# Optimization experiments

Measured on AMD Instinct MI355X. Metric: run time of the kernel, lower is better.

The kernel has to match this reference:

```python
import jax, jax.numpy as jnp
import numpy as np
import math

B, NQ, NK = 4, 2048, 2048
D = 1024          # dimension_k == dimension_v == dimension_q
H, DK, DV = 8, 128, 128
DO = 1024


def setup_inputs() -> dict:
    key = jax.random.key(0)
    ks = jax.random.split(key, 12)
    s = 0.02
    return {
        "q": jax.random.normal(ks[0], (B, NQ, D), jnp.float32),
        "k": jax.random.normal(ks[1], (B, NK, D), jnp.float32),
        "v": jax.random.normal(ks[2], (B, NK, D), jnp.float32),
        "mask": jax.random.normal(ks[3], (B, NQ, NK), jnp.float32),
        "Wq": jax.random.normal(ks[4], (H * DK, D), jnp.float32) * s,
        "bq": jnp.zeros((H * DK,), jnp.float32),
        "Wk": jax.random.normal(ks[5], (DK, D), jnp.float32) * s,
        "bk": jnp.zeros((DK,), jnp.float32),
        "Wv": jax.random.normal(ks[6], (DV, D), jnp.float32) * s,
        "bv": jnp.zeros((DV,), jnp.float32),
        "Wo": jax.random.normal(ks[7], (DO, H * DV), jnp.float32) * s,
        "bo": jnp.zeros((DO,), jnp.float32),
    }


def reference(q, k, v, mask, Wq, bq, Wk, bk, Wv, bv, Wo, bo):
    # projections
    qh = (q @ Wq.T + bq).reshape(B, NQ, H, DK)   # per-head queries
    kh = k @ Wk.T + bk                            # (B, NK, DK) shared across heads (MQA)
    vh = v @ Wv.T + bv                            # (B, NK, DV)
    # scores: shared K broadcast over heads instead of torch's repeat()
    att = jnp.einsum("bqhd,bkd->bhqk", qh, kh) / math.sqrt(DK)
    att = att + mask[:, None, :, :]
    att = jax.nn.softmax(att, axis=-1)
    outh = jnp.einsum("bhqk,bkd->bqhd", att, vh).reshape(B, NQ, H * DV)
    out = outh @ Wo.T + bo
    # original returns attention flattened head-major: (H*B, NQ, NK)
    attention = jnp.transpose(att, (1, 0, 2, 3)).reshape(H * B, NQ, NK)
    return attention, out
```

## Files before the change

kernel.cpp:

```cpp
#include <hip/hip_runtime.h>
#include <cstdint>
#include <cstddef>

typedef unsigned short ushort_t;
typedef __attribute__((ext_vector_type(8))) short short8;
typedef __attribute__((ext_vector_type(4))) float f32x4;
typedef __attribute__((ext_vector_type(4))) unsigned short u16x4;
typedef __attribute__((ext_vector_type(8))) unsigned short u16x8;

#if __has_builtin(__builtin_amdgcn_exp2f)
#define EXP2(x) __builtin_amdgcn_exp2f(x)
#else
#define EXP2(x) exp2f(x)
#endif

__device__ __forceinline__ ushort_t f2b(float f) {
  unsigned u = __builtin_bit_cast(unsigned, f);
  u += 0x7fffu + ((u >> 16) & 1u);
  return (ushort_t)(u >> 16);
}
__device__ __forceinline__ float b2f(ushort_t b) {
  return __builtin_bit_cast(float, (unsigned)b << 16);
}

__device__ __forceinline__ void gload16(const ushort_t* g, ushort_t* lbase, int lane) {
#if __has_builtin(__builtin_amdgcn_global_load_lds)
  __builtin_amdgcn_global_load_lds(
      (const __attribute__((address_space(1))) unsigned int*)(unsigned long long)(const void*)g,
      (__attribute__((address_space(3))) unsigned int*)(unsigned int)(unsigned long long)(void*)lbase,
      16, 0, 0);
#else
  *(u16x8*)((char*)lbase + lane * 16) = *(const u16x8*)g;
#endif
}

#define ATT_ELEMS ((size_t)32 * 2048 * 2048)

enum { MODE_QH = 0, MODE_KV = 1, MODE_OUT = 2 };

__global__ __launch_bounds__(256) void cvt8(const float* __restrict__ in,
                                            ushort_t* __restrict__ out) {
  size_t i = ((size_t)blockIdx.x * 256 + threadIdx.x) * 8;
  f32x4 a = *(const f32x4*)(in + i);
  f32x4 c = *(const f32x4*)(in + i + 4);
  u16x8 o = {f2b(a[0]), f2b(a[1]), f2b(a[2]), f2b(a[3]),
             f2b(c[0]), f2b(c[1]), f2b(c[2]), f2b(c[3])};
  *(u16x8*)(out + i) = o;
}

template <int MODE>
__global__ __launch_bounds__(256) void gemm_bf16(const ushort_t* __restrict__ A,
                                                 const ushort_t* __restrict__ Bw,
                                                 const float* __restrict__ bias,
                                                 void* __restrict__ Cout,
                                                 const ushort_t* __restrict__ A2,
                                                 const ushort_t* __restrict__ B2,
                                                 const float* __restrict__ bias2,
                                                 void* __restrict__ C2) {
  __shared__ __align__(16) ushort_t Alds[128 * 64];
  __shared__ __align__(16) ushort_t Blds[128 * 64];
  if constexpr (MODE == MODE_KV) {
    if (blockIdx.z == 1) { A = A2; Bw = B2; bias = bias2; Cout = C2; }
  }
  const int m0 = blockIdx.x * 128, n0 = blockIdx.y * 128;
  const int t = threadIdx.x, lane = t & 63, w = t >> 6;
  const int quad = lane >> 4, l16 = lane & 15;
  const int wm = w >> 1, wn = w & 1;
  const int lr = lane >> 3;
  const int lc = (lane & 7) * 8;

  f32x4 acc[4][4];
#pragma unroll
  for (int i = 0; i < 4; i++)
#pragma unroll
    for (int j = 0; j < 4; j++) acc[i][j] = (f32x4)0.f;

  for (int k0 = 0; k0 < 1024; k0 += 64) {
    __syncthreads();
#pragma unroll
    for (int c = 0; c < 4; c++) {
      int rbase = w * 32 + c * 8;
      gload16(A + (size_t)(m0 + rbase + lr) * 1024 + k0 + lc, &Alds[rbase * 64], lane);
      gload16(Bw + (size_t)(n0 + rbase + lr) * 1024 + k0 + lc, &Blds[rbase * 64], lane);
    }
    __syncthreads();
#pragma unroll
    for (int ks = 0; ks < 2; ks++) {
      short8 af[4], bfr[4];
#pragma unroll
      for (int mi = 0; mi < 4; mi++)
        af[mi] = *(const short8*)(&Alds[(64 * wm + 16 * mi + l16) * 64 + ks * 32 + quad * 8]);
#pragma unroll
      for (int nj = 0; nj < 4; nj++)
        bfr[nj] = *(const short8*)(&Blds[(64 * wn + 16 * nj + l16) * 64 + ks * 32 + quad * 8]);
#pragma unroll
      for (int mi = 0; mi < 4; mi++)
#pragma unroll
        for (int nj = 0; nj < 4; nj++)
          acc[mi][nj] = __builtin_amdgcn_mfma_f32_16x16x32_bf16(af[mi], bfr[nj], acc[mi][nj], 0, 0, 0);
    }
  }
#pragma unroll
  for (int nj = 0; nj < 4; nj++) {
    int gn = n0 + 64 * wn + 16 * nj + l16;
    float bv = bias[gn];
#pragma unroll
    for (int mi = 0; mi < 4; mi++) {
#pragma unroll
      for (int r = 0; r < 4; r++) {
        int gm = m0 + 64 * wm + 16 * mi + 4 * quad + r;
        float vv = acc[mi][nj][r] + bv;
        if constexpr (MODE == MODE_QH) {
          int bb = gm >> 11, qq = gm & 2047, hh = gn >> 7, dk = gn & 127;
          ((ushort_t*)Cout)[((size_t)((bb * 8 + hh) * 2048 + qq)) * 128 + dk] = f2b(vv);
        } else if constexpr (MODE == MODE_KV) {
          if (blockIdx.z == 0) {
            ((ushort_t*)Cout)[(size_t)gm * 128 + gn] = f2b(vv);
          } else {
            int bb = gm >> 11, nk = gm & 2047;
            ((ushort_t*)Cout)[((size_t)(bb * 128 + gn)) * 2048 + nk] = f2b(vv);
          }
        } else {
          ((float*)Cout)[(size_t)gm * 1024 + gn] = vv;
        }
      }
    }
  }
}

__global__ __launch_bounds__(256, 2) void attn_kernel(const ushort_t* __restrict__ qh,
                                                      const ushort_t* __restrict__ kh,
                                                      const ushort_t* __restrict__ vT,
                                                      const ushort_t* __restrict__ maskb,
                                                      float* __restrict__ att_out,
                                                      ushort_t* __restrict__ outh) {
  __shared__ __align__(16) ushort_t Klds[128 * 136];
  __shared__ __align__(16) ushort_t Vlds[128 * 136];
  const int q0 = blockIdx.x * 128;
  const int h = blockIdx.y, b = blockIdx.z;
  const int t = threadIdx.x, w = t >> 6, lane = t & 63;
  const int quad = lane >> 4, l16 = lane & 15;
  const float SCALE = 0.088388347648318447f;
  const float L2E = 1.4426950408889634f;
  const int srow = t >> 4, scol = (t & 15) * 8;

  short8 aq[2][4];
#pragma unroll
  for (int mi = 0; mi < 2; mi++)
#pragma unroll
    for (int ks = 0; ks < 4; ks++) {
      int qrow = q0 + 32 * w + 16 * mi + l16;
      aq[mi][ks] =
          *(const short8*)(qh + ((size_t)((b * 8 + h) * 2048 + qrow)) * 128 + ks * 32 + quad * 8);
    }

  float m_run[2][4], l_run[2][4];
#pragma unroll
  for (int mi = 0; mi < 2; mi++)
#pragma unroll
    for (int r = 0; r < 4; r++) { m_run[mi][r] = -1e30f; l_run[mi][r] = 0.f; }

  for (int nk0 = 0; nk0 < 2048; nk0 += 128) {
    __syncthreads();
#pragma unroll
    for (int p = 0; p < 8; p++) {
      int r = p * 16 + srow;
      *(u16x8*)(&Klds[r * 136 + scol]) =
          *(const u16x8*)(kh + (size_t)(b * 2048 + nk0 + r) * 128 + scol);
      *(u16x8*)(&Vlds[r * 136 + scol]) =
          *(const u16x8*)(maskb + ((size_t)b * 2048 + q0 + r) * 2048 + nk0 + scol);
    }
    __syncthreads();
    f32x4 acc[2][8];
#pragma unroll
    for (int mi = 0; mi < 2; mi++)
#pragma unroll
      for (int nj = 0; nj < 8; nj++) acc[mi][nj] = (f32x4)0.f;
#pragma unroll
    for (int ks = 0; ks < 4; ks++) {
      short8 bk[8];
#pragma unroll
      for (int nj = 0; nj < 8; nj++)
        bk[nj] = *(const short8*)(&Klds[(16 * nj + l16) * 136 + ks * 32 + quad * 8]);
#pragma unroll
      for (int mi = 0; mi < 2; mi++)
#pragma unroll
        for (int nj = 0; nj < 8; nj++)
          acc[mi][nj] = __builtin_amdgcn_mfma_f32_16x16x32_bf16(aq[mi][ks], bk[nj], acc[mi][nj], 0, 0, 0);
    }
#pragma unroll
    for (int mi = 0; mi < 2; mi++) {
#pragma unroll
      for (int r = 0; r < 4; r++) {
        const int trow = 32 * w + 16 * mi + 4 * quad + r;
        float sv[8];
        float vmax = -1e30f;
#pragma unroll
        for (int nj = 0; nj < 8; nj++) {
          float s = acc[mi][nj][r] * SCALE + b2f(Vlds[trow * 136 + 16 * nj + l16]);
          sv[nj] = s;
          vmax = fmaxf(vmax, s);
        }
#pragma unroll
        for (int o = 1; o < 16; o <<= 1) vmax = fmaxf(vmax, __shfl_xor(vmax, o, 16));
        float mnew = fmaxf(m_run[mi][r], vmax);
        float ssum = 0.f;
#pragma unroll
        for (int nj = 0; nj < 8; nj++) ssum += EXP2((sv[nj] - mnew) * L2E);
#pragma unroll
        for (int o = 1; o < 16; o <<= 1) ssum += __shfl_xor(ssum, o, 16);
        l_run[mi][r] = l_run[mi][r] * EXP2((m_run[mi][r] - mnew) * L2E) + ssum;
        m_run[mi][r] = mnew;
      }
    }
  }

  float rinv[2][4];
#pragma unroll
  for (int mi = 0; mi < 2; mi++)
#pragma unroll
    for (int r = 0; r < 4; r++) rinv[mi][r] = 1.f / l_run[mi][r];

  f32x4 oacc[2][8];
#pragma unroll
  for (int mi = 0; mi < 2; mi++)
#pragma unroll
    for (int nj = 0; nj < 8; nj++) oacc[mi][nj] = (f32x4)0.f;

  for (int nk0 = 0; nk0 < 2048; nk0 += 128) {
    __syncthreads();
#pragma unroll
    for (int p = 0; p < 8; p++) {
      int r = p * 16 + srow;
      *(u16x8*)(&Klds[r * 136 + scol]) =
          *(const u16x8*)(kh + (size_t)(b * 2048 + nk0 + r) * 128 + scol);
      *(u16x8*)(&Vlds[r * 136 + scol]) =
          *(const u16x8*)(maskb + ((size_t)b * 2048 + q0 + r) * 2048 + nk0 + scol);
    }
    __syncthreads();
    f32x4 acc[2][8];
#pragma unroll
    for (int mi = 0; mi < 2; mi++)
#pragma unroll
      for (int nj = 0; nj < 8; nj++) acc[mi][nj] = (f32x4)0.f;
#pragma unroll
    for (int ks = 0; ks < 4; ks++) {
      short8 bk[8];
#pragma unroll
      for (int nj = 0; nj < 8; nj++)
        bk[nj] = *(const short8*)(&Klds[(16 * nj + l16) * 136 + ks * 32 + quad * 8]);
#pragma unroll
      for (int mi = 0; mi < 2; mi++)
#pragma unroll
        for (int nj = 0; nj < 8; nj++)
          acc[mi][nj] = __builtin_amdgcn_mfma_f32_16x16x32_bf16(aq[mi][ks], bk[nj], acc[mi][nj], 0, 0, 0);
    }
#pragma unroll
    for (int mi = 0; mi < 2; mi++) {
#pragma unroll
      for (int r = 0; r < 4; r++) {
        const int trow = 32 * w + 16 * mi + 4 * quad + r;
        const int gq = q0 + trow;
        float* orow = att_out + ((size_t)(h * 4 + b) * 2048 + gq) * 2048 + nk0;
        float mr = m_run[mi][r], ri = rinv[mi][r];
#pragma unroll
        for (int nj = 0; nj < 8; nj++) {
          float s = acc[mi][nj][r] * SCALE + b2f(Vlds[trow * 136 + 16 * nj + l16]);
          float pv = EXP2((s - mr) * L2E) * ri;
          orow[16 * nj + l16] = pv;
          acc[mi][nj][r] = pv;
        }
      }
    }
    __syncthreads();
#pragma unroll
    for (int p = 0; p < 8; p++) {
      int r = p * 16 + srow;
      *(u16x8*)(&Vlds[r * 136 + scol]) =
          *(const u16x8*)(vT + (size_t)(b * 128 + r) * 2048 + nk0 + scol);
    }
#pragma unroll
    for (int mi = 0; mi < 2; mi++) {
#pragma unroll
      for (int r = 0; r < 4; r++) {
        ushort_t* prow = &Klds[(32 * w + 16 * mi + 4 * quad + r) * 136];
#pragma unroll
        for (int nj = 0; nj < 8; nj++) prow[16 * nj + l16] = f2b(acc[mi][nj][r]);
      }
    }
    __syncthreads();
#pragma unroll
    for (int ks = 0; ks < 4; ks++) {
      short8 ap[2], bv[8];
#pragma unroll
      for (int mi = 0; mi < 2; mi++)
        ap[mi] = *(const short8*)(&Klds[(32 * w + 16 * mi + l16) * 136 + ks * 32 + quad * 8]);
#pragma unroll
      for (int nj = 0; nj < 8; nj++)
        bv[nj] = *(const short8*)(&Vlds[(16 * nj + l16) * 136 + ks * 32 + quad * 8]);
#pragma unroll
      for (int mi = 0; mi < 2; mi++)
#pragma unroll
        for (int nj = 0; nj < 8; nj++)
          oacc[mi][nj] = __builtin_amdgcn_mfma_f32_16x16x32_bf16(ap[mi], bv[nj], oacc[mi][nj], 0, 0, 0);
    }
  }
#pragma unroll
  for (int mi = 0; mi < 2; mi++)
#pragma unroll
    for (int nj = 0; nj < 8; nj++)
#pragma unroll
      for (int r = 0; r < 4; r++) {
        int gq = q0 + 32 * w + 16 * mi + 4 * quad + r;
        int dv = 16 * nj + l16;
        outh[(size_t)(b * 2048 + gq) * 1024 + h * 128 + dv] = f2b(oacc[mi][nj][r]);
      }
}

extern "C" void kernel_launch(void* const* d_in, const int* in_sizes, int n_in,
                              void* d_out, int out_size, void* d_ws, size_t ws_size,
                              hipStream_t stream) {
  const float* q    = (const float*)d_in[0];
  const float* k    = (const float*)d_in[1];
  const float* v    = (const float*)d_in[2];
  const float* mask = (const float*)d_in[3];
  const float* Wq   = (const float*)d_in[4];
  const float* bq   = (const float*)d_in[5];
  const float* Wk   = (const float*)d_in[6];
  const float* bk   = (const float*)d_in[7];
  const float* Wv   = (const float*)d_in[8];
  const float* bv   = (const float*)d_in[9];
  const float* Wo   = (const float*)d_in[10];
  const float* bo   = (const float*)d_in[11];

  float* att = (float*)d_out;
  float* out = att + ATT_ELEMS;

  char* ws = (char*)d_ws;
  ushort_t* qh_b   = (ushort_t*)(ws);
  ushort_t* kh_b   = (ushort_t*)(ws + 16777216);
  ushort_t* vT_b   = (ushort_t*)(ws + 18874368);
  ushort_t* outh_b = (ushort_t*)(ws + 20971520);
  ushort_t* mb     = (ushort_t*)(ws + 37748736);

  char* scr = (char*)d_out;
  ushort_t* qb  = (ushort_t*)(scr);
  ushort_t* kb  = (ushort_t*)(scr + 16777216);
  ushort_t* vb  = (ushort_t*)(scr + 33554432);
  ushort_t* Wqb = (ushort_t*)(scr + 50331648);
  ushort_t* Wkb = (ushort_t*)(scr + 52428800);
  ushort_t* Wvb = (ushort_t*)(scr + 52690944);
  ushort_t* Wob = mb;

  cvt8<<<8192, 256, 0, stream>>>(mask, mb);
  cvt8<<<4096, 256, 0, stream>>>(q, qb);
  cvt8<<<4096, 256, 0, stream>>>(k, kb);
  cvt8<<<4096, 256, 0, stream>>>(v, vb);
  cvt8<<<512, 256, 0, stream>>>(Wq, Wqb);
  cvt8<<<64, 256, 0, stream>>>(Wk, Wkb);
  cvt8<<<64, 256, 0, stream>>>(Wv, Wvb);

  gemm_bf16<MODE_QH><<<dim3(64, 8), 256, 0, stream>>>(qb, Wqb, bq, qh_b,
                                                      nullptr, nullptr, nullptr, nullptr);
  gemm_bf16<MODE_KV><<<dim3(64, 1, 2), 256, 0, stream>>>(kb, Wkb, bk, kh_b,
                                                         vb, Wvb, bv, vT_b);
  attn_kernel<<<dim3(16, 8, 4), 256, 0, stream>>>(qh_b, kh_b, vT_b, mb, att, outh_b);
  cvt8<<<512, 256, 0, stream>>>(Wo, Wob);
  gemm_bf16<MODE_OUT><<<dim3(64, 8), 256, 0, stream>>>(outh_b, Wob, bo, out,
                                                       nullptr, nullptr, nullptr, nullptr);
}
```

Before: 1.054 ms.

## Transpose mask to key-major, fold scale into Q, use 8 waves per attention block

The mask is converted to bf16 in transposed (key-major) layout with log2(e) prescaled, so each lane reads its four accumulator rows' mask values as one vector from LDS. The softmax scale and log2(e) are folded into the Q projection epilogue, which removes per-element multiplies. The attention kernel moves from 4 waves of 32 rows each to 8 waves of 16 rows each, with smaller per-thread register arrays. Several small conversion launches are merged into batched kernels. The added transpose pass costs extra LDS work, and the 512-thread launch raises register and occupancy pressure.

```diff
diff --git a/kernel.cpp b/kernel.cpp
--- a/kernel.cpp
+++ b/kernel.cpp
@@ -37,6 +37,8 @@
 #define ATT_ELEMS ((size_t)32 * 2048 * 2048)
 
 enum { MODE_QH = 0, MODE_KV = 1, MODE_OUT = 2 };
+#define QSCALE (0.088388347648318447f * 1.4426950408889634f)
+#define L2E 1.4426950408889634f
 
 __global__ __launch_bounds__(256) void cvt8(const float* __restrict__ in,
                                             ushort_t* __restrict__ out) {
@@ -46,6 +48,60 @@
   u16x8 o = {f2b(a[0]), f2b(a[1]), f2b(a[2]), f2b(a[3]),
              f2b(c[0]), f2b(c[1]), f2b(c[2]), f2b(c[3])};
   *(u16x8*)(out + i) = o;
+}
+
+__global__ __launch_bounds__(256) void cvt8_qkv(const float* __restrict__ q,
+                                                const float* __restrict__ k,
+                                                const float* __restrict__ v,
+                                                ushort_t* __restrict__ oq,
+                                                ushort_t* __restrict__ ok,
+                                                ushort_t* __restrict__ ov) {
+  const float* in = blockIdx.y == 0 ? q : (blockIdx.y == 1 ? k : v);
+  ushort_t* out = blockIdx.y == 0 ? oq : (blockIdx.y == 1 ? ok : ov);
+  size_t i = ((size_t)blockIdx.x * 256 + threadIdx.x) * 8;
+  f32x4 a = *(const f32x4*)(in + i);
+  f32x4 c = *(const f32x4*)(in + i + 4);
+  u16x8 o = {f2b(a[0]), f2b(a[1]), f2b(a[2]), f2b(a[3]),
+             f2b(c[0]), f2b(c[1]), f2b(c[2]), f2b(c[3])};
+  *(u16x8*)(out + i) = o;
+}
+
+__global__ __launch_bounds__(256) void cvt8_wkv(const float* __restrict__ wk,
+                                                const float* __restrict__ wv,
+                                                ushort_t* __restrict__ ok,
+                                                ushort_t* __restrict__ ov) {
+  const float* in = blockIdx.y == 0 ? wk : wv;
+  ushort_t* out = blockIdx.y == 0 ? ok : ov;
+  size_t i = ((size_t)blockIdx.x * 256 + threadIdx.x) * 8;
+  f32x4 a = *(const f32x4*)(in + i);
+  f32x4 c = *(const f32x4*)(in + i + 4);
+  u16x8 o = {f2b(a[0]), f2b(a[1]), f2b(a[2]), f2b(a[3]),
+             f2b(c[0]), f2b(c[1]), f2b(c[2]), f2b(c[3])};
+  *(u16x8*)(out + i) = o;
+}
+
+__global__ __launch_bounds__(256) void cvt_maskT(const float* __restrict__ m,
+                                                 ushort_t* __restrict__ mt) {
+  __shared__ ushort_t tile[64 * 68];
+  const int b = blockIdx.z;
+  const int q0 = blockIdx.y * 64, n0 = blockIdx.x * 64;
+  const int t = threadIdx.x;
+  const int r = t >> 4;
+  const int c4 = (t & 15) * 4;
+#pragma unroll
+  for (int p = 0; p < 4; p++) {
+    int q = p * 16 + r;
+    f32x4 v = *(const f32x4*)(m + ((size_t)b * 2048 + q0 + q) * 2048 + n0 + c4);
+#pragma unroll
+    for (int j = 0; j < 4; j++) tile[(c4 + j) * 68 + q] = f2b(v[j] * L2E);
+  }
+  __syncthreads();
+#pragma unroll
+  for (int p = 0; p < 4; p++) {
+    int nk = p * 16 + r;
+    u16x4 o = *(const u16x4*)(&tile[nk * 68 + c4]);
+    *(u16x4*)(mt + ((size_t)b * 2048 + n0 + nk) * 2048 + q0 + c4) = o;
+  }
 }
 
 template <int MODE>
@@ -111,6 +167,7 @@
         int gm = m0 + 64 * wm + 16 * mi + 4 * quad + r;
         float vv = acc[mi][nj][r] + bv;
         if constexpr (MODE == MODE_QH) {
+          vv *= QSCALE;
           int bb = gm >> 11, qq = gm & 2047, hh = gn >> 7, dk = gn & 127;
           ((ushort_t*)Cout)[((size_t)((bb * 8 + hh) * 2048 + qq)) * 128 + dk] = f2b(vv);
         } else if constexpr (MODE == MODE_KV) {
@@ -128,54 +185,46 @@
   }
 }
 
-__global__ __launch_bounds__(256, 2) void attn_kernel(const ushort_t* __restrict__ qh,
+__global__ __launch_bounds__(512, 4) void attn_kernel(const ushort_t* __restrict__ qh,
                                                       const ushort_t* __restrict__ kh,
                                                       const ushort_t* __restrict__ vT,
-                                                      const ushort_t* __restrict__ maskb,
+                                                      const ushort_t* __restrict__ maskT,
                                                       float* __restrict__ att_out,
                                                       ushort_t* __restrict__ outh) {
   __shared__ __align__(16) ushort_t Klds[128 * 136];
-  __shared__ __align__(16) ushort_t Vlds[128 * 136];
+  __shared__ __align__(16) ushort_t Mlds[128 * 136];
   const int q0 = blockIdx.x * 128;
   const int h = blockIdx.y, b = blockIdx.z;
   const int t = threadIdx.x, w = t >> 6, lane = t & 63;
   const int quad = lane >> 4, l16 = lane & 15;
-  const float SCALE = 0.088388347648318447f;
-  const float L2E = 1.4426950408889634f;
-  const int srow = t >> 4, scol = (t & 15) * 8;
-
-  short8 aq[2][4];
-#pragma unroll
-  for (int mi = 0; mi < 2; mi++)
-#pragma unroll
-    for (int ks = 0; ks < 4; ks++) {
-      int qrow = q0 + 32 * w + 16 * mi + l16;
-      aq[mi][ks] =
-          *(const short8*)(qh + ((size_t)((b * 8 + h) * 2048 + qrow)) * 128 + ks * 32 + quad * 8);
-    }
-
-  float m_run[2][4], l_run[2][4];
-#pragma unroll
-  for (int mi = 0; mi < 2; mi++)
-#pragma unroll
-    for (int r = 0; r < 4; r++) { m_run[mi][r] = -1e30f; l_run[mi][r] = 0.f; }
+  const int srow = t >> 4;
+  const int scol = (t & 15) * 8;
+
+  short8 aq[4];
+#pragma unroll
+  for (int ks = 0; ks < 4; ks++) {
+    int qrow = q0 + 16 * w + l16;
+    aq[ks] = *(const short8*)(qh + ((size_t)((b * 8 + h) * 2048 + qrow)) * 128 + ks * 32 + quad * 8);
+  }
+
+  float m_run[4], l_run[4];
+#pragma unroll
+  for (int r = 0; r < 4; r++) { m_run[r] = -1e30f; l_run[r] = 0.f; }
 
   for (int nk0 = 0; nk0 < 2048; nk0 += 128) {
     __syncthreads();
 #pragma unroll
-    for (int p = 0; p < 8; p++) {
-      int r = p * 16 + srow;
+    for (int p = 0; p < 4; p++) {
+      int r = p * 32 + srow;
       *(u16x8*)(&Klds[r * 136 + scol]) =
           *(const u16x8*)(kh + (size_t)(b * 2048 + nk0 + r) * 128 + scol);
-      *(u16x8*)(&Vlds[r * 136 + scol]) =
-          *(const u16x8*)(maskb + ((size_t)b * 2048 + q0 + r) * 2048 + nk0 + scol);
-    }
-    __syncthreads();
-    f32x4 acc[2][8];
-#pragma unroll
-    for (int mi = 0; mi < 2; mi++)
-#pragma unroll
-      for (int nj = 0; nj < 8; nj++) acc[mi][nj] = (f32x4)0.f;
+      *(u16x8*)(&Mlds[r * 136 + scol]) =
+          *(const u16x8*)(maskT + ((size_t)b * 2048 + nk0 + r) * 2048 + q0 + scol);
+    }
+    __syncthreads();
+    f32x4 acc[8];
+#pragma unroll
+    for (int nj = 0; nj < 8; nj++) acc[nj] = (f32x4)0.f;
 #pragma unroll
     for (int ks = 0; ks < 4; ks++) {
       short8 bk[8];
@@ -183,66 +232,55 @@
       for (int nj = 0; nj < 8; nj++)
         bk[nj] = *(const short8*)(&Klds[(16 * nj + l16) * 136 + ks * 32 + quad * 8]);
 #pragma unroll
-      for (int mi = 0; mi < 2; mi++)
-#pragma unroll
-        for (int nj = 0; nj < 8; nj++)
-          acc[mi][nj] = __builtin_amdgcn_mfma_f32_16x16x32_bf16(aq[mi][ks], bk[nj], acc[mi][nj], 0, 0, 0);
-    }
-#pragma unroll
-    for (int mi = 0; mi < 2; mi++) {
-#pragma unroll
-      for (int r = 0; r < 4; r++) {
-        const int trow = 32 * w + 16 * mi + 4 * quad + r;
-        float sv[8];
-        float vmax = -1e30f;
-#pragma unroll
-        for (int nj = 0; nj < 8; nj++) {
-          float s = acc[mi][nj][r] * SCALE + b2f(Vlds[trow * 136 + 16 * nj + l16]);
-          sv[nj] = s;
-          vmax = fmaxf(vmax, s);
-        }
-#pragma unroll
-        for (int o = 1; o < 16; o <<= 1) vmax = fmaxf(vmax, __shfl_xor(vmax, o, 16));
-        float mnew = fmaxf(m_run[mi][r], vmax);
-        float ssum = 0.f;
-#pragma unroll
-        for (int nj = 0; nj < 8; nj++) ssum += EXP2((sv[nj] - mnew) * L2E);
-#pragma unroll
-        for (int o = 1; o < 16; o <<= 1) ssum += __shfl_xor(ssum, o, 16);
-        l_run[mi][r] = l_run[mi][r] * EXP2((m_run[mi][r] - mnew) * L2E) + ssum;
-        m_run[mi][r] = mnew;
-      }
-    }
-  }
-
-  float rinv[2][4];
-#pragma unroll
-  for (int mi = 0; mi < 2; mi++)
-#pragma unroll
-    for (int r = 0; r < 4; r++) rinv[mi][r] = 1.f / l_run[mi][r];
-
-  f32x4 oacc[2][8];
-#pragma unroll
-  for (int mi = 0; mi < 2; mi++)
-#pragma unroll
-    for (int nj = 0; nj < 8; nj++) oacc[mi][nj] = (f32x4)0.f;
+      for (int nj = 0; nj < 8; nj++)
+        acc[nj] = __builtin_amdgcn_mfma_f32_16x16x32_bf16(aq[ks], bk[nj], acc[nj], 0, 0, 0);
+    }
+#pragma unroll
+    for (int nj = 0; nj < 8; nj++) {
+      u16x4 mv = *(const u16x4*)(&Mlds[(16 * nj + l16) * 136 + 16 * w + 4 * quad]);
+#pragma unroll
+      for (int r = 0; r < 4; r++) acc[nj][r] += b2f(mv[r]);
+    }
+#pragma unroll
+    for (int r = 0; r < 4; r++) {
+      float vmax = acc[0][r];
+#pragma unroll
+      for (int nj = 1; nj < 8; nj++) vmax = fmaxf(vmax, acc[nj][r]);
+#pragma unroll
+      for (int o = 1; o < 16; o <<= 1) vmax = fmaxf(vmax, __shfl_xor(vmax, o, 16));
+      float mnew = fmaxf(m_run[r], vmax);
+      float ssum = 0.f;
+#pragma unroll
+      for (int nj = 0; nj < 8; nj++) ssum += EXP2(acc[nj][r] - mnew);
+#pragma unroll
+      for (int o = 1; o < 16; o <<= 1) ssum += __shfl_xor(ssum, o, 16);
+      l_run[r] = l_run[r] * EXP2(m_run[r] - mnew) + ssum;
+      m_run[r] = mnew;
+    }
+  }
+
+  float rinv[4];
+#pragma unroll
+  for (int r = 0; r < 4; r++) rinv[r] = 1.f / l_run[r];
+
+  f32x4 oacc[8];
+#pragma unroll
+  for (int nj = 0; nj < 8; nj++) oacc[nj] = (f32x4)0.f;
 
   for (int nk0 = 0; nk0 < 2048; nk0 += 128) {
     __syncthreads();
 #pragma unroll
-    for (int p = 0; p < 8; p++) {
-      int r = p * 16 + srow;
+    for (int p = 0; p < 4; p++) {
+      int r = p * 32 + srow;
       *(u16x8*)(&Klds[r * 136 + scol]) =
           *(const u16x8*)(kh + (size_t)(b * 2048 + nk0 + r) * 128 + scol);
-      *(u16x8*)(&Vlds[r * 136 + scol]) =
-          *(const u16x8*)(maskb + ((size_t)b * 2048 + q0 + r) * 2048 + nk0 + scol);
-    }
-    __syncthreads();
-    f32x4 acc[2][8];
-#pragma unroll
-    for (int mi = 0; mi < 2; mi++)
-#pragma unroll
-      for (int nj = 0; nj < 8; nj++) acc[mi][nj] = (f32x4)0.f;
+      *(u16x8*)(&Mlds[r * 136 + scol]) =
+          *(const u16x8*)(maskT + ((size_t)b * 2048 + nk0 + r) * 2048 + q0 + scol);
+    }
+    __syncthreads();
+    f32x4 acc[8];
+#pragma unroll
+    for (int nj = 0; nj < 8; nj++) acc[nj] = (f32x4)0.f;
 #pragma unroll
     for (int ks = 0; ks < 4; ks++) {
       short8 bk[8];
@@ -250,71 +288,57 @@
       for (int nj = 0; nj < 8; nj++)
         bk[nj] = *(const short8*)(&Klds[(16 * nj + l16) * 136 + ks * 32 + quad * 8]);
 #pragma unroll
-      for (int mi = 0; mi < 2; mi++)
-#pragma unroll
-        for (int nj = 0; nj < 8; nj++)
-          acc[mi][nj] = __builtin_amdgcn_mfma_f32_16x16x32_bf16(aq[mi][ks], bk[nj], acc[mi][nj], 0, 0, 0);
-    }
-#pragma unroll
-    for (int mi = 0; mi < 2; mi++) {
-#pragma unroll
-      for (int r = 0; r < 4; r++) {
-        const int trow = 32 * w + 16 * mi + 4 * quad + r;
-        const int gq = q0 + trow;
-        float* orow = att_out + ((size_t)(h * 4 + b) * 2048 + gq) * 2048 + nk0;
-        float mr = m_run[mi][r], ri = rinv[mi][r];
-#pragma unroll
-        for (int nj = 0; nj < 8; nj++) {
-          float s = acc[mi][nj][r] * SCALE + b2f(Vlds[trow * 136 + 16 * nj + l16]);
-          float pv = EXP2((s - mr) * L2E) * ri;
-          orow[16 * nj + l16] = pv;
-          acc[mi][nj][r] = pv;
-        }
-      }
-    }
-    __syncthreads();
-#pragma unroll
-    for (int p = 0; p < 8; p++) {
-      int r = p * 16 + srow;
-      *(u16x8*)(&Vlds[r * 136 + scol]) =
+      for (int nj = 0; nj < 8; nj++)
+        acc[nj] = __builtin_amdgcn_mfma_f32_16x16x32_bf16(aq[ks], bk[nj], acc[nj], 0, 0, 0);
+    }
+#pragma unroll
+    for (int nj = 0; nj < 8; nj++) {
+      u16x4 mv = *(const u16x4*)(&Mlds[(16 * nj + l16) * 136 + 16 * w + 4 * quad]);
+#pragma unroll
+      for (int r = 0; r < 4; r++)
+        acc[nj][r] = EXP2(acc[nj][r] + b2f(mv[r]) - m_run[r]) * rinv[r];
+    }
+#pragma unroll
+    for (int r = 0; r < 4; r++) {
+      int gq = q0 + 16 * w + 4 * quad + r;
+      float* orow = att_out + ((size_t)(h * 4 + b) * 2048 + gq) * 2048 + nk0;
+#pragma unroll
+      for (int nj = 0; nj < 8; nj++) orow[16 * nj + l16] = acc[nj][r];
+    }
+    __syncthreads();
+#pragma unroll
+    for (int p = 0; p < 4; p++) {
+      int r = p * 32 + srow;
+      *(u16x8*)(&Mlds[r * 136 + scol]) =
           *(const u16x8*)(vT + (size_t)(b * 128 + r) * 2048 + nk0 + scol);
     }
 #pragma unroll
-    for (int mi = 0; mi < 2; mi++) {
-#pragma unroll
-      for (int r = 0; r < 4; r++) {
-        ushort_t* prow = &Klds[(32 * w + 16 * mi + 4 * quad + r) * 136];
-#pragma unroll
-        for (int nj = 0; nj < 8; nj++) prow[16 * nj + l16] = f2b(acc[mi][nj][r]);
-      }
+    for (int r = 0; r < 4; r++) {
+      ushort_t* prow = &Klds[(16 * w + 4 * quad + r) * 136];
+#pragma unroll
+      for (int nj = 0; nj < 8; nj++) prow[16 * nj + l16] = f2b(acc[nj][r]);
     }
     __syncthreads();
 #pragma unroll
     for (int ks = 0; ks < 4; ks++) {
-      short8 ap[2], bv[8];
-#pragma unroll
-      for (int mi = 0; mi < 2; mi++)
-        ap[mi] = *(const short8*)(&Klds[(32 * w + 16 * mi + l16) * 136 + ks * 32 + quad * 8]);
-#pragma unroll
-      for (int nj = 0; nj < 8; nj++)
-        bv[nj] = *(const short8*)(&Vlds[(16 * nj + l16) * 136 + ks * 32 + quad * 8]);
-#pragma unroll
-      for (int mi = 0; mi < 2; mi++)
-#pragma unroll
-        for (int nj = 0; nj < 8; nj++)
-          oacc[mi][nj] = __builtin_amdgcn_mfma_f32_16x16x32_bf16(ap[mi], bv[nj], oacc[mi][nj], 0, 0, 0);
-    }
-  }
-#pragma unroll
-  for (int mi = 0; mi < 2; mi++)
-#pragma unroll
-    for (int nj = 0; nj < 8; nj++)
-#pragma unroll
-      for (int r = 0; r < 4; r++) {
-        int gq = q0 + 32 * w + 16 * mi + 4 * quad + r;
-        int dv = 16 * nj + l16;
-        outh[(size_t)(b * 2048 + gq) * 1024 + h * 128 + dv] = f2b(oacc[mi][nj][r]);
-      }
+      short8 ap = *(const short8*)(&Klds[(16 * w + l16) * 136 + ks * 32 + quad * 8]);
+      short8 bv[8];
+#pragma unroll
+      for (int nj = 0; nj < 8; nj++)
+        bv[nj] = *(const short8*)(&Mlds[(16 * nj + l16) * 136 + ks * 32 + quad * 8]);
+#pragma unroll
+      for (int nj = 0; nj < 8; nj++)
+        oacc[nj] = __builtin_amdgcn_mfma_f32_16x16x32_bf16(ap, bv[nj], oacc[nj], 0, 0, 0);
+    }
+  }
+#pragma unroll
+  for (int nj = 0; nj < 8; nj++)
+#pragma unroll
+    for (int r = 0; r < 4; r++) {
+      int gq = q0 + 16 * w + 4 * quad + r;
+      int dv = 16 * nj + l16;
+      outh[(size_t)(b * 2048 + gq) * 1024 + h * 128 + dv] = f2b(oacc[nj][r]);
+    }
 }
 
 extern "C" void kernel_launch(void* const* d_in, const int* in_sizes, int n_in,
@@ -352,19 +376,16 @@
   ushort_t* Wvb = (ushort_t*)(scr + 52690944);
   ushort_t* Wob = mb;
 
-  cvt8<<<8192, 256, 0, stream>>>(mask, mb);
-  cvt8<<<4096, 256, 0, stream>>>(q, qb);
-  cvt8<<<4096, 256, 0, stream>>>(k, kb);
-  cvt8<<<4096, 256, 0, stream>>>(v, vb);
+  cvt_maskT<<<dim3(32, 32, 4), 256, 0, stream>>>(mask, mb);
+  cvt8_qkv<<<dim3(4096, 3), 256, 0, stream>>>(q, k, v, qb, kb, vb);
   cvt8<<<512, 256, 0, stream>>>(Wq, Wqb);
-  cvt8<<<64, 256, 0, stream>>>(Wk, Wkb);
-  cvt8<<<64, 256, 0, stream>>>(Wv, Wvb);
+  cvt8_wkv<<<dim3(64, 2), 256, 0, stream>>>(Wk, Wv, Wkb, Wvb);
 
   gemm_bf16<MODE_QH><<<dim3(64, 8), 256, 0, stream>>>(qb, Wqb, bq, qh_b,
                                                       nullptr, nullptr, nullptr, nullptr);
   gemm_bf16<MODE_KV><<<dim3(64, 1, 2), 256, 0, stream>>>(kb, Wkb, bk, kh_b,
                                                          vb, Wvb, bv, vT_b);
-  attn_kernel<<<dim3(16, 8, 4), 256, 0, stream>>>(qh_b, kh_b, vT_b, mb, att, outh_b);
+  attn_kernel<<<dim3(16, 8, 4), 512, 0, stream>>>(qh_b, kh_b, vT_b, mb, att, outh_b);
   cvt8<<<512, 256, 0, stream>>>(Wo, Wob);
   gemm_bf16<MODE_OUT><<<dim3(64, 8), 256, 0, stream>>>(outh_b, Wob, bo, out,
                                                        nullptr, nullptr, nullptr, nullptr);
```

Result: faster. 994.2 us (-5.7%).
